# Optimization experiments

Measured on AMD Instinct MI355X. Metric: run time of the kernel, lower is better.

Reference implementation:

```python
import jax, jax.numpy as jnp
import numpy as np
from jax import lax

GAMMA = 0.1  # fixed RBF bandwidth from LearnableRBFInfluence


def setup_inputs() -> dict:
    key = jax.random.key(0)
    k1, k2, k3, k4 = jax.random.split(key, 4)
    B, H, W = 2, 256, 256
    NUM_FILTERS, KS, NUM_BASIS = 48, 7, 31
    u_log = jax.random.normal(k1, (B, 1, H, W), jnp.float32)
    f_log = jax.random.normal(k2, (B, 1, H, W), jnp.float32)
    filters = jax.random.normal(k3, (NUM_FILTERS, 1, KS, KS), jnp.float32) * 0.05
    rbf_weights = jax.random.normal(k4, (NUM_FILTERS, NUM_BASIS), jnp.float32) * 0.05
    lambda_param = jnp.float32(0.1)
    return {"u_log": u_log, "f_log": f_log, "filters": filters,
            "rbf_weights": rbf_weights, "lambda_param": lambda_param}


def reference(u_log, f_log, filters, rbf_weights, lambda_param):
    # Batched form of the per-filter loop:
    #   conv[i] = conv2d(u, k_i)  ->  one grouped conv with 48 output channels
    num_basis = rbf_weights.shape[1]
    mu = jnp.linspace(-1.0, 1.0, num_basis).astype(u_log.dtype)  # [K]

    dn = lax.conv_dimension_numbers(u_log.shape, filters.shape, ('NCHW', 'OIHW', 'NCHW'))
    conv = lax.conv_general_dilated(u_log, filters, (1, 1), 'SAME',
                                    dimension_numbers=dn)  # [B,48,H,W]

    # RBF influence, per filter channel c: phi = sum_k w[c,k] * exp(-(conv-mu_k)^2/(2 g^2))
    diff = conv[..., None] - mu                              # [B,48,H,W,K]
    rbf = jnp.exp(-(diff * diff) / (2.0 * GAMMA * GAMMA))
    phi = jnp.einsum('bchwk,ck->bchw', rbf, rbf_weights)     # [B,48,H,W]

    # Per-filter conv2d(phi_i, flip(k_i)) summed over i == single conv
    # with OIHW weight [1,48,7,7] built from spatially-flipped filters.
    kT = jnp.flip(filters, axis=(2, 3)).transpose(1, 0, 2, 3)  # [1,48,7,7]
    dn2 = lax.conv_dimension_numbers(phi.shape, kT.shape, ('NCHW', 'OIHW', 'NCHW'))
    diffusion = lax.conv_general_dilated(phi, kT, (1, 1), 'SAME',
                                         dimension_numbers=dn2)  # [B,1,H,W]

    reaction = lambda_param * (u_log - f_log)
    return u_log - diffusion - reaction
```

## Files before the change

### kernel.cpp

```cpp
#include <hip/hip_runtime.h>

#define HH 256
#define WW 256
#define NPIX (2 * HH * WW)
#define NC 48
#define NB 31
#define OT 32
#define PT 38
#define PSTR 44
#define UT 44
#define USTR 52
#define TP 192


__global__ __launch_bounds__(256)
void tnrd_table(const float* __restrict__ wr, float2* __restrict__ tab)
{
    const int ch = blockIdx.x;
    const float* rc = wr + ch * NB;
    for (int j = threadIdx.x; j < TP; j += 256) {
        float v0 = 0.f, v1 = 0.f;
        float x0 = fmaf((float)j, 1.0f / 64.0f, -1.5f);
        float x1 = x0 + 1.0f / 64.0f;
        #pragma unroll
        for (int k = 0; k < NB; ++k) {
            float mu = -1.f + (float)k * (1.f / 15.f);
            float d0 = x0 - mu, d1 = x1 - mu;
            float w = rc[k];
            v0 = fmaf(w, __expf(-50.f * d0 * d0), v0);
            v1 = fmaf(w, __expf(-50.f * d1 * d1), v1);
        }
        tab[ch * TP + j] = make_float2(v0, v1 - v0);
    }
}

#define F1STEP(WI, s0, s1, s2, s3)                                      \
    { float fa = wa[WI], fb = wb[WI];                                   \
      a0 = fmaf(s0, fa, a0); a1 = fmaf(s1, fa, a1);                     \
      a2 = fmaf(s2, fa, a2); a3 = fmaf(s3, fa, a3);                     \
      b0 = fmaf(s0, fb, b0); b1 = fmaf(s1, fb, b1);                     \
      b2 = fmaf(s2, fb, b2); b3 = fmaf(s3, fb, b3); }

#define F1ROW(WA, WB, q0, q1, q2)                                       \
    { const float* wa = (WA); const float* wb = (WB);                   \
      F1STEP(0, q0.x, q0.y, q0.z, q0.w)                                 \
      F1STEP(1, q0.y, q0.z, q0.w, q1.x)                                 \
      F1STEP(2, q0.z, q0.w, q1.x, q1.y)                                 \
      F1STEP(3, q0.w, q1.x, q1.y, q1.z)                                 \
      F1STEP(4, q1.x, q1.y, q1.z, q1.w)                                 \
      F1STEP(5, q1.y, q1.z, q1.w, q2.x)                                 \
      F1STEP(6, q1.z, q1.w, q2.x, q2.y) }

#define LERP1(res, aval, T)                                             \
    { float t_ = fminf(fmaxf(fmaf(aval, 64.f, 96.f), 0.f), 191.999f);   \
      float fj_ = floorf(t_);                                           \
      float2 e_ = (T)[(int)fj_];               \
      res = fmaf(t_ - fj_, e_.y, e_.x); }

#define C2STEP(WI, s0, s1, s2, s3, t0, t1, t2, t3)                      \
    { float fa = wra[WI], fb = wrb[WI];                                 \
      o0 = fmaf(s0, fa, o0); o1 = fmaf(s1, fa, o1);                     \
      o2 = fmaf(s2, fa, o2); o3 = fmaf(s3, fa, o3);                     \
      o0 = fmaf(t0, fb, o0); o1 = fmaf(t1, fb, o1);                     \
      o2 = fmaf(t2, fb, o2); o3 = fmaf(t3, fb, o3); }

template<int CPG>
__global__ __launch_bounds__(256, 6)
void tnrd_main(const float* __restrict__ u,
               const float* __restrict__ wf,
               const float2* __restrict__ tab,
               float* __restrict__ part)
{
    constexpr int NGRP = NC / CPG;
    constexpr int NPASS = CPG / 2;
    __shared__ __align__(16) float u_s[UT * USTR];
    __shared__ __align__(16) float phi_s[2][PT * PSTR];

    const int tid = threadIdx.x;
    const int bx = blockIdx.x, by = blockIdx.y;
    const int b = blockIdx.z / NGRP, g = blockIdx.z % NGRP;
    const int c0g = g * CPG;

    const int uy0 = by * OT - 6, ux0 = bx * OT - 6;
    const float* ub = u + b * (HH * WW);
    for (int i = tid; i < UT * USTR; i += 256) {
        int r = i / USTR, c = i - r * USTR;
        int gy = uy0 + r, gx = ux0 + c;
        float v = 0.f;
        if (c < UT && (unsigned)gy < HH && (unsigned)gx < WW)
            v = ub[gy * WW + gx];
        u_s[i] = v;
    }
    __syncthreads();

    const int oy = tid >> 3;
    const int ox0 = (tid & 7) * 4;
    float o0 = 0.f, o1 = 0.f, o2 = 0.f, o3 = 0.f;
    const int py0 = by * OT - 3, px0 = bx * OT - 3;

    auto conv1_pass = [&](int cp, float* __restrict__ bufA,
                          float* __restrict__ bufB) {
        const float* wA = wf + (c0g + 2 * cp) * 49;
        const float* wB = wA + 49;
        const float2* tA = tab + (c0g + 2 * cp) * TP;
        const float2* tB = tA + TP;
        for (int p = 0; p < 2; ++p) {
            const int gi = tid + p * 256;
            if (gi < PT * 10) {
                const int pr = gi % PT, pc = (gi / PT) * 4;
                float a0 = 0.f, a1 = 0.f, a2 = 0.f, a3 = 0.f;
                float b0 = 0.f, b1 = 0.f, b2 = 0.f, b3 = 0.f;
                const float* bptr = &u_s[pr * USTR + pc];

                float4 c0 = *(const float4*)(bptr);
                float4 c1 = *(const float4*)(bptr + 4);
                float2 c2 = *(const float2*)(bptr + 8);
                #pragma unroll 1
                for (int dy = 0; dy < 6; ++dy) {
                    const float* nr = bptr + (dy + 1) * USTR;
                    float4 n0 = *(const float4*)(nr);
                    float4 n1 = *(const float4*)(nr + 4);
                    float2 n2 = *(const float2*)(nr + 8);
                    F1ROW(wA + dy * 7, wB + dy * 7, c0, c1, c2)
                    c0 = n0; c1 = n1; c2 = n2;
                }
                F1ROW(wA + 42, wB + 42, c0, c1, c2)

                const int gy = py0 + pr;
                const bool rowok = (unsigned)gy < HH;
                const bool ok0 = rowok && (unsigned)(px0 + pc + 0) < WW;
                const bool ok1 = rowok && (unsigned)(px0 + pc + 1) < WW;
                const bool ok2 = rowok && (unsigned)(px0 + pc + 2) < WW;
                const bool ok3 = rowok && (unsigned)(px0 + pc + 3) < WW;
                float pA0, pA1, pA2, pA3, pB0, pB1, pB2, pB3;
                LERP1(pA0, a0, tA) LERP1(pB0, b0, tB)
                LERP1(pA1, a1, tA) LERP1(pB1, b1, tB)
                LERP1(pA2, a2, tA) LERP1(pB2, b2, tB)
                LERP1(pA3, a3, tA) LERP1(pB3, b3, tB)
                pA0 = ok0 ? pA0 : 0.f;  pB0 = ok0 ? pB0 : 0.f;
                pA1 = ok1 ? pA1 : 0.f;  pB1 = ok1 ? pB1 : 0.f;
                pA2 = ok2 ? pA2 : 0.f;  pB2 = ok2 ? pB2 : 0.f;
                pA3 = ok3 ? pA3 : 0.f;  pB3 = ok3 ? pB3 : 0.f;
                *(float4*)(bufA + pr * PSTR + pc) =
                    make_float4(pA0, pA1, pA2, pA3);
                *(float4*)(bufB + pr * PSTR + pc) =
                    make_float4(pB0, pB1, pB2, pB3);
            }
        }
    };

    #pragma unroll 1
    for (int pass = 0; pass < NPASS; ++pass) {
        conv1_pass(pass, phi_s[0], phi_s[1]);
        __syncthreads();

        const float* wA = wf + (c0g + 2 * pass) * 49;
        const float* wB = wA + 49;
        const float* pA = phi_s[0];
        const float* pB = phi_s[1];
        for (int dy = 0; dy < 7; ++dy) {
            const float* rA = pA + (oy + dy) * PSTR + ox0;
            const float* rB = pB + (oy + dy) * PSTR + ox0;
            const float4 A0 = *(const float4*)(rA);
            const float4 A1 = *(const float4*)(rA + 4);
            const float2 A2 = *(const float2*)(rA + 8);
            const float4 B0 = *(const float4*)(rB);
            const float4 B1 = *(const float4*)(rB + 4);
            const float2 B2 = *(const float2*)(rB + 8);
            const float* wra = wA + (6 - dy) * 7;
            const float* wrb = wB + (6 - dy) * 7;
            C2STEP(6, A0.x, A0.y, A0.z, A0.w, B0.x, B0.y, B0.z, B0.w)
            C2STEP(5, A0.y, A0.z, A0.w, A1.x, B0.y, B0.z, B0.w, B1.x)
            C2STEP(4, A0.z, A0.w, A1.x, A1.y, B0.z, B0.w, B1.x, B1.y)
            C2STEP(3, A0.w, A1.x, A1.y, A1.z, B0.w, B1.x, B1.y, B1.z)
            C2STEP(2, A1.x, A1.y, A1.z, A1.w, B1.x, B1.y, B1.z, B1.w)
            C2STEP(1, A1.y, A1.z, A1.w, A2.x, B1.y, B1.z, B1.w, B2.x)
            C2STEP(0, A1.z, A1.w, A2.x, A2.y, B1.z, B1.w, B2.x, B2.y)
        }
        if (pass < NPASS - 1) __syncthreads();
    }

    const int gy = by * OT + oy, gx = bx * OT + ox0;
    float4 v4 = make_float4(o0, o1, o2, o3);
    *reinterpret_cast<float4*>(part + (size_t)g * NPIX + b * (HH * WW)
                               + gy * WW + gx) = v4;
}

template<int NGRP>
__global__ __launch_bounds__(256)
void combine_kernel(const float* __restrict__ u,
                    const float* __restrict__ f,
                    const float* __restrict__ lam,
                    const float* __restrict__ part,
                    float* __restrict__ out)
{
    int i = blockIdx.x * 256 + threadIdx.x;
    float d = 0.f;
    #pragma unroll
    for (int g = 0; g < NGRP; ++g) d += part[g * NPIX + i];
    float lv = lam[0];
    float uv = u[i];
    float fv = f[i];
    out[i] = uv - d - lv * (uv - fv);
}

extern "C" void kernel_launch(void* const* d_in, const int* in_sizes, int n_in,
                              void* d_out, int out_size, void* d_ws, size_t ws_size,
                              hipStream_t stream) {
    const float* u    = (const float*)d_in[0];
    const float* f    = (const float*)d_in[1];
    const float* filt = (const float*)d_in[2];
    const float* rbfw = (const float*)d_in[3];
    const float* lam  = (const float*)d_in[4];
    float* out = (float*)d_out;
    float* part = (float*)d_ws;
    float2* tabg = (float2*)d_out;

    tnrd_table<<<NC, 256, 0, stream>>>(rbfw, tabg);
    if (ws_size >= (size_t)24 * NPIX * sizeof(float)) {
        tnrd_main<2><<<dim3(8, 8, 48), 256, 0, stream>>>(u, filt, tabg, part);
        combine_kernel<24><<<512, 256, 0, stream>>>(u, f, lam, part, out);
    } else if (ws_size >= (size_t)12 * NPIX * sizeof(float)) {
        tnrd_main<4><<<dim3(8, 8, 24), 256, 0, stream>>>(u, filt, tabg, part);
        combine_kernel<12><<<512, 256, 0, stream>>>(u, f, lam, part, out);
    } else {
        tnrd_main<8><<<dim3(8, 8, 12), 256, 0, stream>>>(u, filt, tabg, part);
        combine_kernel<6><<<512, 256, 0, stream>>>(u, f, lam, part, out);
    }
}
```

Measured before the change: 104.6 us.

## Use wider 32x64 tiles with two output rows per thread in main kernel

Adds a specialized main kernel for the two-channel-per-group path. It uses 32x64 output tiles so the halo recompute of the first convolution and the input load are amortized over more pixels. In the second convolution each thread computes two output rows, so every loaded phi row serves both. The cost is more shared memory and registers per block, with occupancy lowered to 4 blocks per SM, and half as many blocks in the grid.

```diff
diff --git a/kernel.cpp b/kernel.cpp
--- a/kernel.cpp
+++ b/kernel.cpp
@@ -5,12 +5,23 @@
 #define NPIX (2 * HH * WW)
 #define NC 48
 #define NB 31
+#define TP 192
+
+#define OTY 32
+#define OTX 64
+#define PTY 38
+#define PTX 70
+#define PSTR2 76
+#define UTY 44
+#define UTX 76
+#define USTR2 84
+#define N1ITEM 684
+
 #define OT 32
 #define PT 38
 #define PSTR 44
 #define UT 44
 #define USTR 52
-#define TP 192
 
 
 __global__ __launch_bounds__(256)
@@ -57,6 +68,140 @@
       float2 e_ = (T)[(int)fj_];               \
       res = fmaf(t_ - fj_, e_.y, e_.x); }
 
+#define C2STEPG(WI, s0, s1, s2, s3, t0, t1, t2, t3)                     \
+    { float fa = wra[WI], fb = wrb[WI];                                 \
+      q0 = fmaf(s0, fa, q0); q1 = fmaf(s1, fa, q1);                     \
+      q2 = fmaf(s2, fa, q2); q3 = fmaf(s3, fa, q3);                     \
+      q0 = fmaf(t0, fb, q0); q1 = fmaf(t1, fb, q1);                     \
+      q2 = fmaf(t2, fb, q2); q3 = fmaf(t3, fb, q3); }
+
+#define C2SWEEP()                                                       \
+    C2STEPG(6, A0.x, A0.y, A0.z, A0.w, B0.x, B0.y, B0.z, B0.w)          \
+    C2STEPG(5, A0.y, A0.z, A0.w, A1.x, B0.y, B0.z, B0.w, B1.x)          \
+    C2STEPG(4, A0.z, A0.w, A1.x, A1.y, B0.z, B0.w, B1.x, B1.y)          \
+    C2STEPG(3, A0.w, A1.x, A1.y, A1.z, B0.w, B1.x, B1.y, B1.z)          \
+    C2STEPG(2, A1.x, A1.y, A1.z, A1.w, B1.x, B1.y, B1.z, B1.w)          \
+    C2STEPG(1, A1.y, A1.z, A1.w, A2.x, B1.y, B1.z, B1.w, B2.x)          \
+    C2STEPG(0, A1.z, A1.w, A2.x, A2.y, B1.z, B1.w, B2.x, B2.y)
+
+__global__ __launch_bounds__(256, 4)
+void tnrd_main_2x(const float* __restrict__ u,
+                  const float* __restrict__ wf,
+                  const float2* __restrict__ tab,
+                  float* __restrict__ part)
+{
+    __shared__ __align__(16) float u_s[UTY * USTR2];
+    __shared__ __align__(16) float phi_s[2][PTY * PSTR2];
+
+    const int tid = threadIdx.x;
+    const int bx = blockIdx.x, by = blockIdx.y;
+    const int b = blockIdx.z / 24, g = blockIdx.z % 24;
+    const int c0 = g * 2;
+
+    const int uy0 = by * OTY - 6, ux0 = bx * OTX - 6;
+    const float* ub = u + b * (HH * WW);
+    for (int i = tid; i < UTY * USTR2; i += 256) {
+        int r = i / USTR2, c = i - r * USTR2;
+        int gy = uy0 + r, gx = ux0 + c;
+        float v = 0.f;
+        if (c < UTX && (unsigned)gy < HH && (unsigned)gx < WW)
+            v = ub[gy * WW + gx];
+        u_s[i] = v;
+    }
+    __syncthreads();
+
+    const int py0 = by * OTY - 3, px0 = bx * OTX - 3;
+
+    {
+        const float* wA = wf + c0 * 49;
+        const float* wB = wA + 49;
+        const float2* tA = tab + c0 * TP;
+        const float2* tB = tA + TP;
+        for (int p = 0; p < 3; ++p) {
+            const int gi = tid + p * 256;
+            if (gi < N1ITEM) {
+                const int pr = gi % PTY, pc = (gi / PTY) * 4;
+                float a0 = 0.f, a1 = 0.f, a2 = 0.f, a3 = 0.f;
+                float b0 = 0.f, b1 = 0.f, b2 = 0.f, b3 = 0.f;
+                const float* bptr = &u_s[pr * USTR2 + pc];
+
+                float4 c0v = *(const float4*)(bptr);
+                float4 c1v = *(const float4*)(bptr + 4);
+                float2 c2v = *(const float2*)(bptr + 8);
+                #pragma unroll 1
+                for (int dy = 0; dy < 6; ++dy) {
+                    const float* nr = bptr + (dy + 1) * USTR2;
+                    float4 n0 = *(const float4*)(nr);
+                    float4 n1 = *(const float4*)(nr + 4);
+                    float2 n2 = *(const float2*)(nr + 8);
+                    F1ROW(wA + dy * 7, wB + dy * 7, c0v, c1v, c2v)
+                    c0v = n0; c1v = n1; c2v = n2;
+                }
+                F1ROW(wA + 42, wB + 42, c0v, c1v, c2v)
+
+                const int gy = py0 + pr;
+                const bool rowok = (unsigned)gy < HH;
+                const bool ok0 = rowok && (unsigned)(px0 + pc + 0) < WW;
+                const bool ok1 = rowok && (unsigned)(px0 + pc + 1) < WW;
+                const bool ok2 = rowok && (unsigned)(px0 + pc + 2) < WW;
+                const bool ok3 = rowok && (unsigned)(px0 + pc + 3) < WW;
+                float pA0, pA1, pA2, pA3, pB0, pB1, pB2, pB3;
+                LERP1(pA0, a0, tA) LERP1(pB0, b0, tB)
+                LERP1(pA1, a1, tA) LERP1(pB1, b1, tB)
+                LERP1(pA2, a2, tA) LERP1(pB2, b2, tB)
+                LERP1(pA3, a3, tA) LERP1(pB3, b3, tB)
+                pA0 = ok0 ? pA0 : 0.f;  pB0 = ok0 ? pB0 : 0.f;
+                pA1 = ok1 ? pA1 : 0.f;  pB1 = ok1 ? pB1 : 0.f;
+                pA2 = ok2 ? pA2 : 0.f;  pB2 = ok2 ? pB2 : 0.f;
+                pA3 = ok3 ? pA3 : 0.f;  pB3 = ok3 ? pB3 : 0.f;
+                *(float4*)(&phi_s[0][pr * PSTR2 + pc]) =
+                    make_float4(pA0, pA1, pA2, pA3);
+                *(float4*)(&phi_s[1][pr * PSTR2 + pc]) =
+                    make_float4(pB0, pB1, pB2, pB3);
+            }
+        }
+    }
+    __syncthreads();
+
+    {
+        const int tr = tid >> 4;
+        const int ox = (tid & 15) * 4;
+        const float* wA = wf + c0 * 49;
+        const float* wB = wA + 49;
+        float o00 = 0.f, o01 = 0.f, o02 = 0.f, o03 = 0.f;
+        float o10 = 0.f, o11 = 0.f, o12 = 0.f, o13 = 0.f;
+
+        #pragma unroll
+        for (int dyt = 0; dyt < 8; ++dyt) {
+            const float* rA = &phi_s[0][(2 * tr + dyt) * PSTR2 + ox];
+            const float* rB = &phi_s[1][(2 * tr + dyt) * PSTR2 + ox];
+            const float4 A0 = *(const float4*)(rA);
+            const float4 A1 = *(const float4*)(rA + 4);
+            const float2 A2 = *(const float2*)(rA + 8);
+            const float4 B0 = *(const float4*)(rB);
+            const float4 B1 = *(const float4*)(rB + 4);
+            const float2 B2 = *(const float2*)(rB + 8);
+            if (dyt < 7) {
+                const float* wra = wA + (6 - dyt) * 7;
+                const float* wrb = wB + (6 - dyt) * 7;
+                float &q0 = o00, &q1 = o01, &q2 = o02, &q3 = o03;
+                C2SWEEP()
+            }
+            if (dyt > 0) {
+                const float* wra = wA + (7 - dyt) * 7;
+                const float* wrb = wB + (7 - dyt) * 7;
+                float &q0 = o10, &q1 = o11, &q2 = o12, &q3 = o13;
+                C2SWEEP()
+            }
+        }
+
+        const int gy0 = by * OTY + 2 * tr, gx = bx * OTX + ox;
+        float* dst = part + (size_t)g * NPIX + b * (HH * WW) + gy0 * WW + gx;
+        *reinterpret_cast<float4*>(dst)      = make_float4(o00, o01, o02, o03);
+        *reinterpret_cast<float4*>(dst + WW) = make_float4(o10, o11, o12, o13);
+    }
+}
+
 #define C2STEP(WI, s0, s1, s2, s3, t0, t1, t2, t3)                      \
     { float fa = wra[WI], fb = wrb[WI];                                 \
       o0 = fmaf(s0, fa, o0); o1 = fmaf(s1, fa, o1);                     \
@@ -111,7 +256,6 @@
                 float a0 = 0.f, a1 = 0.f, a2 = 0.f, a3 = 0.f;
                 float b0 = 0.f, b1 = 0.f, b2 = 0.f, b3 = 0.f;
                 const float* bptr = &u_s[pr * USTR + pc];
-
                 float4 c0 = *(const float4*)(bptr);
                 float4 c1 = *(const float4*)(bptr + 4);
                 float2 c2 = *(const float2*)(bptr + 8);
@@ -125,7 +269,6 @@
                     c0 = n0; c1 = n1; c2 = n2;
                 }
                 F1ROW(wA + 42, wB + 42, c0, c1, c2)
-
                 const int gy = py0 + pr;
                 const bool rowok = (unsigned)gy < HH;
                 const bool ok0 = rowok && (unsigned)(px0 + pc + 0) < WW;
@@ -153,7 +296,6 @@
     for (int pass = 0; pass < NPASS; ++pass) {
         conv1_pass(pass, phi_s[0], phi_s[1]);
         __syncthreads();
-
         const float* wA = wf + (c0g + 2 * pass) * 49;
         const float* wB = wA + 49;
         const float* pA = phi_s[0];
@@ -218,7 +360,8 @@
 
     tnrd_table<<<NC, 256, 0, stream>>>(rbfw, tabg);
     if (ws_size >= (size_t)24 * NPIX * sizeof(float)) {
-        tnrd_main<2><<<dim3(8, 8, 48), 256, 0, stream>>>(u, filt, tabg, part);
+        tnrd_main_2x<<<dim3(WW / OTX, HH / OTY, 48), 256, 0, stream>>>(
+            u, filt, tabg, part);
         combine_kernel<24><<<512, 256, 0, stream>>>(u, f, lam, part, out);
     } else if (ws_size >= (size_t)12 * NPIX * sizeof(float)) {
         tnrd_main<4><<<dim3(8, 8, 24), 256, 0, stream>>>(u, filt, tabg, part);
```

After: 100.1 us. -4.3%, faster.
